# Performance work log

Measured on AMD Instinct MI355X. Metric: run time of the kernel, lower is better.

The kernel has to match this reference:

```python
import jax, jax.numpy as jnp
import numpy as np

D_MODEL = 2048
NUM_HEADS = 16
D_K = D_MODEL // NUM_HEADS  # 128
THETA = 10000.0
BATCH = 2
SEQ = 2048


def _rope(v, pos):
    # v: [..., S, d_k], pos: [..., S] int
    half = v.shape[-1] // 2
    inv_freq = THETA ** (-(jnp.arange(half, dtype=jnp.float32) * 2.0) / v.shape[-1])
    ang = pos[..., None].astype(jnp.float32) * inv_freq  # [..., S, half]
    cos, sin = jnp.cos(ang), jnp.sin(ang)
    x1 = v[..., 0::2]
    x2 = v[..., 1::2]
    r1 = x1 * cos - x2 * sin
    r2 = x1 * sin + x2 * cos
    return jnp.stack([r1, r2], axis=-1).reshape(v.shape)


def setup_inputs() -> dict:
    key = jax.random.key(0)
    ks = jax.random.split(key, 5)
    scale = D_MODEL ** -0.5
    x = jax.random.normal(ks[0], (BATCH, SEQ, D_MODEL), dtype=jnp.float32)
    WQ = jax.random.normal(ks[1], (D_MODEL, D_MODEL), dtype=jnp.float32) * scale
    WK = jax.random.normal(ks[2], (D_MODEL, D_MODEL), dtype=jnp.float32) * scale
    WV = jax.random.normal(ks[3], (D_MODEL, D_MODEL), dtype=jnp.float32) * scale
    WO = jax.random.normal(ks[4], (D_MODEL, D_MODEL), dtype=jnp.float32) * scale
    token_positions = jnp.broadcast_to(jnp.arange(SEQ, dtype=jnp.int32), (BATCH, SEQ))
    return {"x": x, "token_positions": token_positions, "WQ": WQ, "WK": WK, "WV": WV, "WO": WO}


def reference(x, token_positions, WQ, WK, WV, WO):
    B, S, _ = x.shape
    split = lambda t: t.reshape(B, S, NUM_HEADS, D_K).transpose(0, 2, 1, 3)  # [B,H,S,d]
    Q = split(x @ WQ.T)
    K = split(x @ WK.T)
    V = split(x @ WV.T)
    pos = token_positions[:, None, :]  # broadcast over heads
    Q = _rope(Q, pos)
    K = _rope(K, pos)
    scores = jnp.einsum('bhqd,bhkd->bhqk', Q, K) / np.sqrt(D_K).astype(np.float32)
    causal = jnp.arange(S)[:, None] >= jnp.arange(S)[None, :]  # [S,S]
    scores = jnp.where(causal, scores, -jnp.inf)
    attn = jax.nn.softmax(scores, axis=-1)
    out = jnp.einsum('bhqk,bhkd->bhqd', attn, V)
    out = out.transpose(0, 2, 1, 3).reshape(B, S, D_MODEL)
    return out @ WO.T
```

## Files before the change

kernel.cpp:

```cpp
#include <hip/hip_runtime.h>

typedef unsigned short ushort;
typedef __attribute__((ext_vector_type(8))) __bf16 bf16x8;
typedef __attribute__((ext_vector_type(8))) ushort ushort8;
typedef __attribute__((ext_vector_type(4))) float f32x4;
typedef __attribute__((ext_vector_type(16))) float f32x16;
typedef __attribute__((ext_vector_type(4))) unsigned u32x4;

#define DM 2048
#define NH 16
#define DK 128
#define BATCH 2
#define SEQ 2048
#define MROWS (BATCH*SEQ)

#define GLDS16(g, l) __builtin_amdgcn_global_load_lds(                         \
    (const __attribute__((address_space(1))) void*)(g),                        \
    (__attribute__((address_space(3))) void*)(l), 16, 0, 0)

__device__ __forceinline__ ushort f2bf(float f) {
  unsigned u = __builtin_bit_cast(unsigned, f);
  u += 0x7fffu + ((u >> 16) & 1u);
  return (ushort)(u >> 16);
}

__device__ __forceinline__ unsigned cvtpk(float lo, float hi) {
  unsigned r;
  asm("v_cvt_pk_bf16_f32 %0, %1, %2" : "=v"(r) : "v"(lo), "v"(hi));
  return r;
}

__global__ __launch_bounds__(256) void cvt_all(const float* __restrict__ x,
                                               const float* __restrict__ w0,
                                               const float* __restrict__ w1,
                                               const float* __restrict__ w2,
                                               const float* __restrict__ w3,
                                               ushort* __restrict__ xb,
                                               ushort* __restrict__ o0,
                                               ushort* __restrict__ o1,
                                               ushort* __restrict__ o2,
                                               ushort* __restrict__ o3) {
  int b = blockIdx.x;
  const float* src;
  ushort* dst;
  int lb;
  if (b < 4096) { src = x; dst = xb; lb = b; }
  else {
    int wsel = (b - 4096) >> 11;
    lb = (b - 4096) & 2047;
    src = (wsel == 0) ? w0 : (wsel == 1) ? w1 : (wsel == 2) ? w2 : w3;
    dst = (wsel == 0) ? o0 : (wsel == 1) ? o1 : (wsel == 2) ? o2 : o3;
  }
  int i = lb * 256 + threadIdx.x;
  const float4* p = (const float4*)src;
  float4 a = p[2 * i], bq = p[2 * i + 1];
  ushort8 o;
  o[0] = f2bf(a.x); o[1] = f2bf(a.y); o[2] = f2bf(a.z); o[3] = f2bf(a.w);
  o[4] = f2bf(bq.x); o[5] = f2bf(bq.y); o[6] = f2bf(bq.z); o[7] = f2bf(bq.w);
  *(ushort8*)(dst + (size_t)8 * i) = o;
}

template <int MODE>
__device__ __forceinline__ void gemm8_body(const ushort* __restrict__ A,
                                           const ushort* __restrict__ Bm,
                                           ushort* __restrict__ obf,
                                           float* __restrict__ ofp,
                                           int row0, int col0) {
  extern __shared__ ushort lds[];
  constexpr int NT = DM / 64;
  const int tid = threadIdx.x;
  const int wid = tid >> 6, lane = tid & 63;
  const int l15 = lane & 15, lhi = lane >> 4;
  const int wm = wid >> 2, wn = wid & 3;
  const int swz = l15 & 7;

  f32x4 acc[8][2];
  const f32x4 z4 = {0.f, 0.f, 0.f, 0.f};
#pragma unroll
  for (int m = 0; m < 8; ++m) { acc[m][0] = z4; acc[m][1] = z4; }

  auto stageA = [&](int kt, int h) {
    ushort* dst = &lds[(kt % 3) * 24576 + h * 8192 + wid * 512];
    const ushort* srcb = A + (size_t)(row0 + h * 128) * DM + kt * 64;
#pragma unroll
    for (int j = 0; j < 2; ++j) {
      int idx = j * 512 + tid;
      int r = idx >> 3, c = idx & 7;
      GLDS16(srcb + (size_t)r * DM + ((c ^ (r & 7)) * 8), dst + j * 4096);
    }
  };
  auto stageB = [&](int kt) {
    ushort* dst = &lds[(kt % 3) * 24576 + 16384 + wid * 512];
    const ushort* srcb = Bm + (size_t)col0 * DM + kt * 64;
#pragma unroll
    for (int j = 0; j < 2; ++j) {
      int idx = j * 512 + tid;
      int r = idx >> 3, c = idx & 7;
      GLDS16(srcb + (size_t)r * DM + ((c ^ (r & 7)) * 8), dst + j * 4096);
    }
  };

  stageA(0, 0); stageA(0, 1); stageB(0);
  stageA(1, 0); stageA(1, 1); stageB(1);
  asm volatile("s_waitcnt vmcnt(6)" ::: "memory");
  __builtin_amdgcn_s_barrier();

  for (int t = 0; t < NT; ++t) {
    const ushort* Ab = &lds[(t % 3) * 24576];
    const ushort* Bb = Ab + 16384;
    const bool pf = (t + 2 < NT);
    bf16x8 bfr[2][2];
#pragma unroll
    for (int p = 0; p < 4; ++p) {
      const int hm = p & 1, ks = p >> 1;
      bf16x8 af[4];
#pragma unroll
      for (int mq = 0; mq < 4; ++mq) {
        int row = wm * 128 + hm * 64 + mq * 16 + l15;
        af[mq] = *(const bf16x8*)&Ab[row * 64 + (((ks * 4 + lhi) ^ swz) * 8)];
      }
      if (hm == 0) {
#pragma unroll
        for (int n = 0; n < 2; ++n) {
          int row = wn * 32 + n * 16 + l15;
          bfr[ks][n] = *(const bf16x8*)&Bb[row * 64 + (((ks * 4 + lhi) ^ swz) * 8)];
        }
      }
      if (pf) {
        if (p == 0) stageA(t + 2, 0);
        else if (p == 1) stageA(t + 2, 1);
        else if (p == 2) stageB(t + 2);
      }
      __builtin_amdgcn_s_barrier();
      __builtin_amdgcn_s_setprio(1);
#pragma unroll
      for (int mq = 0; mq < 4; ++mq)
#pragma unroll
        for (int n = 0; n < 2; ++n)
          acc[hm * 4 + mq][n] = __builtin_amdgcn_mfma_f32_16x16x32_bf16(
              af[mq], bfr[ks][n], acc[hm * 4 + mq][n], 0, 0, 0);
      __builtin_amdgcn_s_setprio(0);
      if (p == 3) {
        if (pf) asm volatile("s_waitcnt vmcnt(6)" ::: "memory");
        else asm volatile("s_waitcnt vmcnt(0)" ::: "memory");
      }
      __builtin_amdgcn_s_barrier();
    }
  }

#pragma unroll
  for (int m = 0; m < 8; ++m) {
    int grow = row0 + wm * 128 + m * 16 + lhi * 4;
#pragma unroll
    for (int n = 0; n < 2; ++n) {
      int gcol = col0 + wn * 32 + n * 16 + l15;
#pragma unroll
      for (int j = 0; j < 4; ++j) {
        float v = acc[m][n][j];
        int r = grow + j;
        if (MODE == 0) {
          int b = r >> 11, s = r & (SEQ - 1);
          int h = gcol >> 7, d = gcol & (DK - 1);
          obf[((size_t)(b * NH + h) * SEQ + s) * DK + d] = f2bf(v);
        } else {
          ofp[(size_t)r * DM + gcol] = v;
        }
      }
    }
  }
}

__global__ __launch_bounds__(512, 2) void gemm8_qkv(const ushort* __restrict__ A,
                                                    const ushort* __restrict__ W0,
                                                    const ushort* __restrict__ W1,
                                                    const ushort* __restrict__ W2,
                                                    ushort* __restrict__ O0,
                                                    ushort* __restrict__ O1,
                                                    ushort* __restrict__ O2) {
  int f = ((int)blockIdx.x & 7) * 96 + ((int)blockIdx.x >> 3);
  int z = f >> 8, rem = f & 255;
  int row0 = (rem >> 4) * 256, col0 = (rem & 15) * 128;
  const ushort* Bm = (z == 0) ? W0 : ((z == 1) ? W1 : W2);
  ushort* obf = (z == 0) ? O0 : ((z == 1) ? O1 : O2);
  gemm8_body<0>(A, Bm, obf, nullptr, row0, col0);
}

__global__ __launch_bounds__(512, 2) void gemm8_out(const ushort* __restrict__ A,
                                                    const ushort* __restrict__ Bm,
                                                    float* __restrict__ ofp) {
  int f = ((int)blockIdx.x & 7) * 32 + ((int)blockIdx.x >> 3);
  int row0 = (f >> 4) * 256, col0 = (f & 15) * 128;
  gemm8_body<1>(A, Bm, nullptr, ofp, row0, col0);
}

__global__ __launch_bounds__(256) void rope_kernel(ushort* __restrict__ buf,
                                                   const int* __restrict__ tpos) {
  int idx = blockIdx.x * 256 + threadIdx.x;
  int c = idx & 15;
  int row = idx >> 4;
  int s = row & (SEQ - 1);
  int bh = row >> 11;
  int b = bh >> 4;
  int pos = tpos[b * SEQ + s];
  int d0 = c * 8;
  ushort8 v = *(ushort8*)(buf + (size_t)row * DK + d0);
  float fp = (float)pos;
#pragma unroll
  for (int p = 0; p < 4; ++p) {
    int i = (d0 >> 1) + p;
    float freq = exp2f(-13.287712379549449f * ((float)i * (1.0f / 64.0f)));
    float ang = fp * freq;
    float sn, cs;
    sincosf(ang, &sn, &cs);
    float x1 = __builtin_bit_cast(float, (unsigned)v[2 * p] << 16);
    float x2 = __builtin_bit_cast(float, (unsigned)v[2 * p + 1] << 16);
    float r1 = x1 * cs - x2 * sn;
    float r2 = x1 * sn + x2 * cs;
    v[2 * p] = f2bf(r1);
    v[2 * p + 1] = f2bf(r2);
  }
  *(ushort8*)(buf + (size_t)row * DK + d0) = v;
}

__global__ __launch_bounds__(256) void transpose_v(const ushort* __restrict__ Vb,
                                                   ushort* __restrict__ Vt) {
  __shared__ ushort t[64 * 80];
  int s0 = blockIdx.x * 64, d0 = blockIdx.y * 64, bh = blockIdx.z;
  const size_t base = (size_t)bh * SEQ * DK;
  int tid = threadIdx.x;
#pragma unroll
  for (int it = 0; it < 2; ++it) {
    int c = it * 256 + tid;
    int r = c >> 3, c8 = (c & 7) * 8;
    ushort8 v = *(const ushort8*)&Vb[base + (size_t)(s0 + r) * DK + d0 + c8];
    *(ushort8*)&t[r * 80 + c8] = v;
  }
  __syncthreads();
  const size_t obase = (size_t)bh * DK * SEQ;
#pragma unroll
  for (int it = 0; it < 2; ++it) {
    int c = it * 256 + tid;
    int dr = c >> 3, sc = (c & 7) * 8;
    ushort8 v;
#pragma unroll
    for (int i2 = 0; i2 < 8; ++i2) v[i2] = t[(sc + i2) * 80 + dr];
    *(ushort8*)&Vt[obase + (size_t)(d0 + dr) * SEQ + s0 + sc] = v;
  }
}

__global__ __launch_bounds__(256, 2) void attn_kernel(const ushort* __restrict__ Qb,
                                                      const ushort* __restrict__ Kb,
                                                      const ushort* __restrict__ Vt,
                                                      ushort* __restrict__ attnb) {
  __shared__ ushort lds[32768];
  const int bx = blockIdx.x;
  const int u = bx & 255, hg = bx >> 8;
  const int qt = hg ? (15 - (u & 15)) : (u & 15);
  const int bh = (u >> 4) + hg * 16;
  const int tid = threadIdx.x;
  const int w = tid >> 6, lane = tid & 63;
  const int l31 = lane & 31, hi = lane >> 5;
  const int qb = qt * 128;
  const int qsb = qb + w * 32;
  const int q = qsb + l31;
  const size_t qk_base = (size_t)bh * SEQ * DK;
  const size_t v_base = (size_t)bh * DK * SEQ;
  const int nt = (qb + 128) >> 6;

  bf16x8 qf[8];
#pragma unroll
  for (int ks = 0; ks < 8; ++ks)
    qf[ks] = *(const bf16x8*)&Qb[qk_base + (size_t)q * DK + ks * 16 + hi * 8];

  f32x16 acc[4];
#pragma unroll
  for (int dt = 0; dt < 4; ++dt)
#pragma unroll
    for (int r = 0; r < 16; ++r) acc[dt][r] = 0.f;

  float m2 = -INFINITY, lsum = 0.f;
  const float cs2 = 0.08838834764831845f * 1.4426950408889634f;

  auto stage = [&](int t, int bufsel) {
    const int kb0 = t * 64;
#pragma unroll
    for (int i = 0; i < 4; ++i) {
      int g = w * 256 + i * 64 + lane;
      int row = g >> 4, c16 = g & 15;
      GLDS16(Kb + qk_base + (size_t)(kb0 + row) * DK + ((c16 ^ (row & 7)) * 8),
             &lds[bufsel * 8192 + (w * 256 + i * 64) * 8]);
    }
#pragma unroll
    for (int i = 0; i < 4; ++i) {
      int g = w * 256 + i * 64 + lane;
      int row = g >> 3, c8 = g & 7;
      GLDS16(Vt + v_base + (size_t)row * SEQ + kb0 + ((c8 ^ (row & 7)) * 8),
             &lds[16384 + bufsel * 8192 + (w * 256 + i * 64) * 8]);
    }
  };

  stage(0, 0);
  __syncthreads();
  int buf = 0;

  for (int t = 0; t < nt; ++t) {
    if (t + 1 < nt) stage(t + 1, buf ^ 1);
    const int kb0 = t * 64;
    if (kb0 <= qsb) {
      const ushort* lk = &lds[buf * 8192];
      const ushort* lv = &lds[16384 + buf * 8192];
      const int kb1 = kb0 + 32;
      const bool diag0 = (kb0 == qsb);
      const bool have1 = (kb1 <= qsb);
      const bool diag1 = (kb1 == qsb);
      const int sw = l31 & 7;

      f32x16 s0, s1;
#pragma unroll
      for (int r = 0; r < 16; ++r) { s0[r] = 0.f; s1[r] = 0.f; }
      __builtin_amdgcn_s_setprio(1);
#pragma unroll
      for (int ks = 0; ks < 8; ++ks) {
        int g = 2 * ks + hi;
        bf16x8 kf = *(const bf16x8*)&lk[(l31 * 16 + (g ^ sw)) * 8];
        s0 = __builtin_amdgcn_mfma_f32_32x32x16_bf16(kf, qf[ks], s0, 0, 0, 0);
      }
      if (have1) {
#pragma unroll
        for (int ks = 0; ks < 8; ++ks) {
          int g = 2 * ks + hi;
          bf16x8 kf = *(const bf16x8*)&lk[((32 + l31) * 16 + (g ^ sw)) * 8];
          s1 = __builtin_amdgcn_mfma_f32_32x32x16_bf16(kf, qf[ks], s1, 0, 0, 0);
        }
      }
      __builtin_amdgcn_s_setprio(0);

      float mx = -INFINITY;
#pragma unroll
      for (int r = 0; r < 16; ++r) {
        float v = s0[r] * cs2;
        if (diag0) {
          int kk = kb0 + (r & 3) + 8 * (r >> 2) + 4 * hi;
          if (kk > q) v = -INFINITY;
        }
        s0[r] = v;
        mx = fmaxf(mx, v);
      }
      if (have1) {
#pragma unroll
        for (int r = 0; r < 16; ++r) {
          float v = s1[r] * cs2;
          if (diag1) {
            int kk = kb1 + (r & 3) + 8 * (r >> 2) + 4 * hi;
            if (kk > q) v = -INFINITY;
          }
          s1[r] = v;
          mx = fmaxf(mx, v);
        }
      }
      mx = fmaxf(mx, __shfl_xor(mx, 32));

      float sc = 1.f;
      if (!__all(mx <= m2 + 11.5f)) {
        float mnew = fmaxf(m2, mx);
        sc = exp2f(m2 - mnew);
        m2 = mnew;
#pragma unroll
        for (int dt = 0; dt < 4; ++dt)
#pragma unroll
          for (int r = 0; r < 16; ++r) acc[dt][r] *= sc;
      }
      float rs = 0.f;
#pragma unroll
      for (int r = 0; r < 16; ++r) {
        float p = exp2f(s0[r] - m2);
        s0[r] = p;
        rs += p;
      }
      if (have1) {
#pragma unroll
        for (int r = 0; r < 16; ++r) {
          float p = exp2f(s1[r] - m2);
          s1[r] = p;
          rs += p;
        }
      }
      rs += __shfl_xor(rs, 32);
      lsum = lsum * sc + rs;

      unsigned w0[8], ws0[8];
#pragma unroll
      for (int i = 0; i < 8; ++i) w0[i] = cvtpk(s0[2 * i], s0[2 * i + 1]);
#pragma unroll
      for (int i = 0; i < 8; ++i) ws0[i] = (unsigned)__shfl_xor((int)w0[i], 32);
      u32x4 b00, b01;
      b00[0] = hi ? ws0[2] : w0[0]; b00[1] = hi ? ws0[3] : w0[1];
      b00[2] = hi ? w0[2] : ws0[0]; b00[3] = hi ? w0[3] : ws0[1];
      b01[0] = hi ? ws0[6] : w0[4]; b01[1] = hi ? ws0[7] : w0[5];
      b01[2] = hi ? w0[6] : ws0[4]; b01[3] = hi ? w0[7] : ws0[5];
      bf16x8 pb00 = __builtin_bit_cast(bf16x8, b00);
      bf16x8 pb01 = __builtin_bit_cast(bf16x8, b01);
      bf16x8 pb10, pb11;
      if (have1) {
        unsigned w1[8], ws1[8];
#pragma unroll
        for (int i = 0; i < 8; ++i) w1[i] = cvtpk(s1[2 * i], s1[2 * i + 1]);
#pragma unroll
        for (int i = 0; i < 8; ++i) ws1[i] = (unsigned)__shfl_xor((int)w1[i], 32);
        u32x4 b10, b11;
        b10[0] = hi ? ws1[2] : w1[0]; b10[1] = hi ? ws1[3] : w1[1];
        b10[2] = hi ? w1[2] : ws1[0]; b10[3] = hi ? w1[3] : ws1[1];
        b11[0] = hi ? ws1[6] : w1[4]; b11[1] = hi ? ws1[7] : w1[5];
        b11[2] = hi ? w1[6] : ws1[4]; b11[3] = hi ? w1[7] : ws1[5];
        pb10 = __builtin_bit_cast(bf16x8, b10);
        pb11 = __builtin_bit_cast(bf16x8, b11);
      }

      __builtin_amdgcn_s_setprio(1);
#pragma unroll
      for (int dt = 0; dt < 4; ++dt) {
        int vr = (dt * 32 + l31) * 8;
        bf16x8 vf0 = *(const bf16x8*)&lv[(vr + ((0 + hi) ^ sw)) * 8];
        bf16x8 vf1 = *(const bf16x8*)&lv[(vr + ((2 + hi) ^ sw)) * 8];
        acc[dt] = __builtin_amdgcn_mfma_f32_32x32x16_bf16(vf0, pb00, acc[dt], 0, 0, 0);
        acc[dt] = __builtin_amdgcn_mfma_f32_32x32x16_bf16(vf1, pb01, acc[dt], 0, 0, 0);
        if (have1) {
          bf16x8 vf2 = *(const bf16x8*)&lv[(vr + ((4 + hi) ^ sw)) * 8];
          bf16x8 vf3 = *(const bf16x8*)&lv[(vr + ((6 + hi) ^ sw)) * 8];
          acc[dt] = __builtin_amdgcn_mfma_f32_32x32x16_bf16(vf2, pb10, acc[dt], 0, 0, 0);
          acc[dt] = __builtin_amdgcn_mfma_f32_32x32x16_bf16(vf3, pb11, acc[dt], 0, 0, 0);
        }
      }
      __builtin_amdgcn_s_setprio(0);
    }
    __syncthreads();
    buf ^= 1;
  }

  ushort* eo = &lds[w * 32 * 136];
  float inv = 1.0f / lsum;
#pragma unroll
  for (int dt = 0; dt < 4; ++dt)
#pragma unroll
    for (int rq = 0; rq < 4; ++rq) {
      unsigned lo = cvtpk(acc[dt][4 * rq] * inv, acc[dt][4 * rq + 1] * inv);
      unsigned hh = cvtpk(acc[dt][4 * rq + 2] * inv, acc[dt][4 * rq + 3] * inv);
      uint2 pr; pr.x = lo; pr.y = hh;
      *(uint2*)&eo[l31 * 136 + dt * 32 + rq * 8 + hi * 4] = pr;
    }
  const int b = bh >> 4, h = bh & (NH - 1);
#pragma unroll
  for (int it = 0; it < 8; ++it) {
    int row = it * 4 + (lane >> 4);
    int c8 = (lane & 15) * 8;
    ushort8 v = *(const ushort8*)&eo[row * 136 + c8];
    *(ushort8*)&attnb[((size_t)b * SEQ + qsb + row) * DM + h * DK + c8] = v;
  }
}

extern "C" void kernel_launch(void* const* d_in, const int* in_sizes, int n_in,
                              void* d_out, int out_size, void* d_ws, size_t ws_size,
                              hipStream_t stream) {
  const float* x = (const float*)d_in[0];
  const int* tpos = (const int*)d_in[1];
  const float* WQ = (const float*)d_in[2];
  const float* WK = (const float*)d_in[3];
  const float* WV = (const float*)d_in[4];
  const float* WO = (const float*)d_in[5];
  float* out = (float*)d_out;
  char* ws = (char*)d_ws;

  ushort* xb  = (ushort*)(ws + 0);
  ushort* wqb = (ushort*)(ws + 16777216);
  ushort* wkb = (ushort*)(ws + 25165824);
  ushort* wvb = (ushort*)(ws + 33554432);
  ushort* wob = (ushort*)(ws + 41943040);
  ushort* Qb  = (ushort*)(ws + 50331648);
  ushort* Kb  = (ushort*)(ws + 67108864);
  ushort* Vb  = (ushort*)(ws + 83886080);
  ushort* Vt  = (ushort*)(ws + 0);
  ushort* attnb = (ushort*)(ws + 16777216);

  hipFuncSetAttribute(reinterpret_cast<const void*>(gemm8_qkv),
                      hipFuncAttributeMaxDynamicSharedMemorySize, 147456);
  hipFuncSetAttribute(reinterpret_cast<const void*>(gemm8_out),
                      hipFuncAttributeMaxDynamicSharedMemorySize, 147456);

  cvt_all<<<12288, 256, 0, stream>>>(x, WQ, WK, WV, WO, xb, wqb, wkb, wvb, wob);

  gemm8_qkv<<<768, 512, 147456, stream>>>(xb, wqb, wkb, wvb, Qb, Kb, Vb);

  rope_kernel<<<4096, 256, 0, stream>>>(Qb, tpos);
  rope_kernel<<<4096, 256, 0, stream>>>(Kb, tpos);

  transpose_v<<<dim3(SEQ / 64, DK / 64, BATCH * NH), 256, 0, stream>>>(Vb, Vt);

  attn_kernel<<<dim3(512), 256, 0, stream>>>(Qb, Kb, Vt, attnb);

  gemm8_out<<<256, 512, 147456, stream>>>(attnb, wob, out);
}
```

Measured before the change: 277.6 us.

## Fuse QKV weights into one GEMM tile sharing A loads, double-buffer pipeline

The QKV GEMM now computes a 128-row tile against all three weight matrices in one block, so each A tile is loaded once and reused for Q, K and V. The pipeline changes from a triple-buffered, phase-interleaved schedule to a simpler double buffer with a full vmcnt(0) wait and barrier every k-step. The output GEMM switches to 128x256 tiles, and the two RoPE launches are merged into one. This cuts A-operand traffic and a launch, but the simpler pipeline may expose more load latency and the larger per-wave accumulator set raises register pressure.

```diff
diff --git a/kernel.cpp b/kernel.cpp
--- a/kernel.cpp
+++ b/kernel.cpp
@@ -60,142 +60,146 @@
   *(ushort8*)(dst + (size_t)8 * i) = o;
 }
 
-template <int MODE>
-__device__ __forceinline__ void gemm8_body(const ushort* __restrict__ A,
-                                           const ushort* __restrict__ Bm,
-                                           ushort* __restrict__ obf,
+template <int NW, int NFR, int MODE>
+__device__ __forceinline__ void gemmF_body(const ushort* __restrict__ A,
+                                           const ushort* __restrict__ B0,
+                                           const ushort* __restrict__ B1,
+                                           const ushort* __restrict__ B2,
+                                           ushort* __restrict__ O0,
+                                           ushort* __restrict__ O1,
+                                           ushort* __restrict__ O2,
                                            float* __restrict__ ofp,
                                            int row0, int col0) {
   extern __shared__ ushort lds[];
   constexpr int NT = DM / 64;
+  constexpr int BUFSZ = 8192 + NW * NFR * 4096;
+  const ushort* Bw[3] = {B0, B1, B2};
+  ushort* Ow[3] = {O0, O1, O2};
   const int tid = threadIdx.x;
   const int wid = tid >> 6, lane = tid & 63;
   const int l15 = lane & 15, lhi = lane >> 4;
   const int wm = wid >> 2, wn = wid & 3;
   const int swz = l15 & 7;
 
-  f32x4 acc[8][2];
+  f32x4 acc[4][NW * NFR];
   const f32x4 z4 = {0.f, 0.f, 0.f, 0.f};
 #pragma unroll
-  for (int m = 0; m < 8; ++m) { acc[m][0] = z4; acc[m][1] = z4; }
-
-  auto stageA = [&](int kt, int h) {
-    ushort* dst = &lds[(kt % 3) * 24576 + h * 8192 + wid * 512];
-    const ushort* srcb = A + (size_t)(row0 + h * 128) * DM + kt * 64;
+  for (int mq = 0; mq < 4; ++mq)
+#pragma unroll
+    for (int i = 0; i < NW * NFR; ++i) acc[mq][i] = z4;
+
+  auto stage = [&](int kt, int buf) {
+    ushort* dstA = &lds[buf * BUFSZ];
+    const ushort* srcA = A + (size_t)row0 * DM + kt * 64;
 #pragma unroll
     for (int j = 0; j < 2; ++j) {
-      int idx = j * 512 + tid;
-      int r = idx >> 3, c = idx & 7;
-      GLDS16(srcb + (size_t)r * DM + ((c ^ (r & 7)) * 8), dst + j * 4096);
+      int g = j * 512 + tid;
+      int r = g >> 3, c = g & 7;
+      GLDS16(srcA + (size_t)r * DM + ((c ^ (r & 7)) * 8),
+             &dstA[(j * 512 + wid * 64) * 8]);
+    }
+#pragma unroll
+    for (int w3 = 0; w3 < NW; ++w3) {
+      ushort* dstB = &lds[buf * BUFSZ + 8192 + w3 * NFR * 4096];
+      const ushort* srcB = Bw[w3] + (size_t)col0 * DM + kt * 64;
+#pragma unroll
+      for (int j = 0; j < NFR; ++j) {
+        int g = j * 512 + tid;
+        int r = g >> 3, c = g & 7;
+        GLDS16(srcB + (size_t)r * DM + ((c ^ (r & 7)) * 8),
+               &dstB[(j * 512 + wid * 64) * 8]);
+      }
     }
   };
-  auto stageB = [&](int kt) {
-    ushort* dst = &lds[(kt % 3) * 24576 + 16384 + wid * 512];
-    const ushort* srcb = Bm + (size_t)col0 * DM + kt * 64;
-#pragma unroll
-    for (int j = 0; j < 2; ++j) {
-      int idx = j * 512 + tid;
-      int r = idx >> 3, c = idx & 7;
-      GLDS16(srcb + (size_t)r * DM + ((c ^ (r & 7)) * 8), dst + j * 4096);
-    }
-  };
-
-  stageA(0, 0); stageA(0, 1); stageB(0);
-  stageA(1, 0); stageA(1, 1); stageB(1);
-  asm volatile("s_waitcnt vmcnt(6)" ::: "memory");
-  __builtin_amdgcn_s_barrier();
+
+  stage(0, 0);
+  asm volatile("s_waitcnt vmcnt(0)" ::: "memory");
+  asm volatile("s_barrier" ::: "memory");
 
   for (int t = 0; t < NT; ++t) {
-    const ushort* Ab = &lds[(t % 3) * 24576];
-    const ushort* Bb = Ab + 16384;
-    const bool pf = (t + 2 < NT);
-    bf16x8 bfr[2][2];
-#pragma unroll
-    for (int p = 0; p < 4; ++p) {
-      const int hm = p & 1, ks = p >> 1;
+    const int cb = t & 1;
+    const ushort* Ab = &lds[cb * BUFSZ];
+    const ushort* Bb = Ab + 8192;
+    if (t + 1 < NT) stage(t + 1, cb ^ 1);
+#pragma unroll
+    for (int ks = 0; ks < 2; ++ks) {
       bf16x8 af[4];
 #pragma unroll
       for (int mq = 0; mq < 4; ++mq) {
-        int row = wm * 128 + hm * 64 + mq * 16 + l15;
+        int row = wm * 64 + mq * 16 + l15;
         af[mq] = *(const bf16x8*)&Ab[row * 64 + (((ks * 4 + lhi) ^ swz) * 8)];
       }
-      if (hm == 0) {
-#pragma unroll
-        for (int n = 0; n < 2; ++n) {
-          int row = wn * 32 + n * 16 + l15;
-          bfr[ks][n] = *(const bf16x8*)&Bb[row * 64 + (((ks * 4 + lhi) ^ swz) * 8)];
-        }
-      }
-      if (pf) {
-        if (p == 0) stageA(t + 2, 0);
-        else if (p == 1) stageA(t + 2, 1);
-        else if (p == 2) stageB(t + 2);
-      }
-      __builtin_amdgcn_s_barrier();
+      bf16x8 bfr[NW * NFR];
+#pragma unroll
+      for (int w3 = 0; w3 < NW; ++w3)
+#pragma unroll
+        for (int n = 0; n < NFR; ++n) {
+          int row = wn * (NFR * 16) + n * 16 + l15;
+          bfr[w3 * NFR + n] =
+              *(const bf16x8*)&Bb[w3 * NFR * 4096 + row * 64 + (((ks * 4 + lhi) ^ swz) * 8)];
+        }
       __builtin_amdgcn_s_setprio(1);
 #pragma unroll
       for (int mq = 0; mq < 4; ++mq)
 #pragma unroll
-        for (int n = 0; n < 2; ++n)
-          acc[hm * 4 + mq][n] = __builtin_amdgcn_mfma_f32_16x16x32_bf16(
-              af[mq], bfr[ks][n], acc[hm * 4 + mq][n], 0, 0, 0);
+        for (int i = 0; i < NW * NFR; ++i)
+          acc[mq][i] = __builtin_amdgcn_mfma_f32_16x16x32_bf16(af[mq], bfr[i], acc[mq][i], 0, 0, 0);
       __builtin_amdgcn_s_setprio(0);
-      if (p == 3) {
-        if (pf) asm volatile("s_waitcnt vmcnt(6)" ::: "memory");
-        else asm volatile("s_waitcnt vmcnt(0)" ::: "memory");
-      }
-      __builtin_amdgcn_s_barrier();
-    }
-  }
-
-#pragma unroll
-  for (int m = 0; m < 8; ++m) {
-    int grow = row0 + wm * 128 + m * 16 + lhi * 4;
-#pragma unroll
-    for (int n = 0; n < 2; ++n) {
-      int gcol = col0 + wn * 32 + n * 16 + l15;
-#pragma unroll
-      for (int j = 0; j < 4; ++j) {
-        float v = acc[m][n][j];
-        int r = grow + j;
-        if (MODE == 0) {
-          int b = r >> 11, s = r & (SEQ - 1);
-          int h = gcol >> 7, d = gcol & (DK - 1);
-          obf[((size_t)(b * NH + h) * SEQ + s) * DK + d] = f2bf(v);
-        } else {
-          ofp[(size_t)r * DM + gcol] = v;
-        }
-      }
-    }
-  }
-}
-
-__global__ __launch_bounds__(512, 2) void gemm8_qkv(const ushort* __restrict__ A,
+    }
+    asm volatile("s_waitcnt vmcnt(0)" ::: "memory");
+    asm volatile("s_barrier" ::: "memory");
+  }
+
+#pragma unroll
+  for (int mq = 0; mq < 4; ++mq) {
+    int grow = row0 + wm * 64 + mq * 16 + lhi * 4;
+#pragma unroll
+    for (int w3 = 0; w3 < NW; ++w3)
+#pragma unroll
+      for (int n = 0; n < NFR; ++n) {
+        int gcol = col0 + wn * (NFR * 16) + n * 16 + l15;
+#pragma unroll
+        for (int j = 0; j < 4; ++j) {
+          float v = acc[mq][w3 * NFR + n][j];
+          int r = grow + j;
+          if (MODE == 0) {
+            int b = r >> 11, s = r & (SEQ - 1);
+            int h = gcol >> 7, d = gcol & (DK - 1);
+            Ow[w3][((size_t)(b * NH + h) * SEQ + s) * DK + d] = f2bf(v);
+          } else {
+            ofp[(size_t)r * DM + gcol] = v;
+          }
+        }
+      }
+  }
+}
+
+__global__ __launch_bounds__(512, 2) void gemmF_qkv(const ushort* __restrict__ A,
                                                     const ushort* __restrict__ W0,
                                                     const ushort* __restrict__ W1,
                                                     const ushort* __restrict__ W2,
                                                     ushort* __restrict__ O0,
                                                     ushort* __restrict__ O1,
                                                     ushort* __restrict__ O2) {
-  int f = ((int)blockIdx.x & 7) * 96 + ((int)blockIdx.x >> 3);
-  int z = f >> 8, rem = f & 255;
-  int row0 = (rem >> 4) * 256, col0 = (rem & 15) * 128;
-  const ushort* Bm = (z == 0) ? W0 : ((z == 1) ? W1 : W2);
-  ushort* obf = (z == 0) ? O0 : ((z == 1) ? O1 : O2);
-  gemm8_body<0>(A, Bm, obf, nullptr, row0, col0);
-}
-
-__global__ __launch_bounds__(512, 2) void gemm8_out(const ushort* __restrict__ A,
+  int f = ((int)blockIdx.x & 7) * 64 + ((int)blockIdx.x >> 3);
+  int row0 = (f >> 4) * 128, col0 = (f & 15) * 128;
+  gemmF_body<3, 2, 0>(A, W0, W1, W2, O0, O1, O2, nullptr, row0, col0);
+}
+
+__global__ __launch_bounds__(512, 2) void gemmF_out(const ushort* __restrict__ A,
                                                     const ushort* __restrict__ Bm,
                                                     float* __restrict__ ofp) {
   int f = ((int)blockIdx.x & 7) * 32 + ((int)blockIdx.x >> 3);
-  int row0 = (f >> 4) * 256, col0 = (f & 15) * 128;
-  gemm8_body<1>(A, Bm, nullptr, ofp, row0, col0);
-}
-
-__global__ __launch_bounds__(256) void rope_kernel(ushort* __restrict__ buf,
+  int row0 = (f >> 3) * 128, col0 = (f & 7) * 256;
+  gemmF_body<1, 4, 1>(A, Bm, nullptr, nullptr, nullptr, nullptr, nullptr, ofp, row0, col0);
+}
+
+__global__ __launch_bounds__(256) void rope_kernel(ushort* __restrict__ Q,
+                                                   ushort* __restrict__ K,
                                                    const int* __restrict__ tpos) {
-  int idx = blockIdx.x * 256 + threadIdx.x;
+  int bid = blockIdx.x;
+  ushort* buf = (bid & 1) ? K : Q;
+  int idx = (bid >> 1) * 256 + threadIdx.x;
   int c = idx & 15;
   int row = idx >> 4;
   int s = row & (SEQ - 1);
@@ -481,21 +485,20 @@
   ushort* Vt  = (ushort*)(ws + 0);
   ushort* attnb = (ushort*)(ws + 16777216);
 
-  hipFuncSetAttribute(reinterpret_cast<const void*>(gemm8_qkv),
-                      hipFuncAttributeMaxDynamicSharedMemorySize, 147456);
-  hipFuncSetAttribute(reinterpret_cast<const void*>(gemm8_out),
-                      hipFuncAttributeMaxDynamicSharedMemorySize, 147456);
+  hipFuncSetAttribute(reinterpret_cast<const void*>(gemmF_qkv),
+                      hipFuncAttributeMaxDynamicSharedMemorySize, 131072);
+  hipFuncSetAttribute(reinterpret_cast<const void*>(gemmF_out),
+                      hipFuncAttributeMaxDynamicSharedMemorySize, 98304);
 
   cvt_all<<<12288, 256, 0, stream>>>(x, WQ, WK, WV, WO, xb, wqb, wkb, wvb, wob);
 
-  gemm8_qkv<<<768, 512, 147456, stream>>>(xb, wqb, wkb, wvb, Qb, Kb, Vb);
-
-  rope_kernel<<<4096, 256, 0, stream>>>(Qb, tpos);
-  rope_kernel<<<4096, 256, 0, stream>>>(Kb, tpos);
+  gemmF_qkv<<<512, 512, 131072, stream>>>(xb, wqb, wkb, wvb, Qb, Kb, Vb);
+
+  rope_kernel<<<8192, 256, 0, stream>>>(Qb, Kb, tpos);
 
   transpose_v<<<dim3(SEQ / 64, DK / 64, BATCH * NH), 256, 0, stream>>>(Vb, Vt);
 
   attn_kernel<<<dim3(512), 256, 0, stream>>>(Qb, Kb, Vt, attnb);
 
-  gemm8_out<<<256, 512, 147456, stream>>>(attnb, wob, out);
-}
+  gemmF_out<<<256, 512, 98304, stream>>>(attnb, wob, out);
+}
```

Measured after the change: 257.7 us. 7.1% less time.
